# Kernel tuning notes

Measured on AMD Instinct MI355X. Metric: run time of the kernel, lower is better.

## Reference

```python
import jax, jax.numpy as jnp
import numpy as np


def _hard_sigmoid(x):
    # Keras ConvLSTM2D default recurrent_activation
    return jnp.clip(0.2 * x + 0.5, 0.0, 1.0)


def _conv(x, w):
    # NHWC input, HWIO kernel, SAME padding, stride 1
    return jax.lax.conv_general_dilated(
        x, w, (1, 1), 'SAME', dimension_numbers=('NHWC', 'HWIO', 'NHWC'))


def _convlstm(seq, h, c, k, rk, b):
    # seq: [B, T, H, W, Cin]; h, c: [B, H, W, F]
    # k: [kh, kw, Cin, 4F], rk: [kh, kw, F, 4F], b: [4F]
    def step(carry, x):
        h, c = carry
        z = _conv(x, k) + _conv(h, rk) + b  # [B,H,W,4F]
        zi, zf, zc, zo = jnp.split(z, 4, axis=-1)
        i = _hard_sigmoid(zi)
        f = _hard_sigmoid(zf)
        o = _hard_sigmoid(zo)
        c = f * c + i * jnp.tanh(zc)
        h = o * jnp.tanh(c)
        return (h, c), None
    (h, c), _ = jax.lax.scan(step, (h, c), jnp.swapaxes(seq, 0, 1))
    return h, c


def setup_inputs() -> dict:
    key = jax.random.key(0)
    ks = jax.random.split(key, 14)
    B, T, H, W, Cin, F, K = 32, 1, 64, 64, 1, 64, 3
    s = 0.05
    inp = {
        'input_': jax.random.normal(ks[0], (B, T, H, W, Cin), jnp.float32),
        'h0': jax.random.normal(ks[1], (B, H, W, F), jnp.float32) * s,
        'c0': jax.random.normal(ks[2], (B, H, W, F), jnp.float32) * s,
        'h1': jax.random.normal(ks[3], (B, H, W, F), jnp.float32) * s,
        'c1': jax.random.normal(ks[4], (B, H, W, F), jnp.float32) * s,
        'k0': jax.random.normal(ks[5], (K, K, Cin, 4 * F), jnp.float32) * s,
        'rk0': jax.random.normal(ks[6], (K, K, F, 4 * F), jnp.float32) * s,
        'b0': jnp.zeros((4 * F,), jnp.float32),
        'k1': jax.random.normal(ks[7], (K, K, F, 4 * F), jnp.float32) * s,
        'rk1': jax.random.normal(ks[8], (K, K, F, 4 * F), jnp.float32) * s,
        'b1': jnp.zeros((4 * F,), jnp.float32),
        'cw': jax.random.normal(ks[9], (1, 1, F, 1), jnp.float32) * s,
        'cb': jnp.zeros((1,), jnp.float32),
    }
    return inp


def reference(input_, h0, c0, h1, c1, k0, rk0, b0, k1, rk1, b1, cw, cb):
    # Layer 0 consumes the input frame sequence (T=1)
    h0n, c0n = _convlstm(input_, h0, c0, k0, rk0, b0)
    # Layer 1 consumes layer-0's last hidden state as its (length-1) input
    h1n, c1n = _convlstm(h0n[:, None], h1, c1, k1, rk1, b1)
    frames = _conv(h1n, cw) + cb  # 1x1 conv head -> [B,H,W,1]
    return frames, h0n, c0n, h1n, c1n
```

## Files before the change

kernel.cpp:

```cpp
#include <hip/hip_runtime.h>
#include <hip/hip_bf16.h>

typedef short s16;
typedef __attribute__((ext_vector_type(8))) short bf16x8;
typedef __attribute__((ext_vector_type(4))) float f32x4;

__device__ __forceinline__ s16 f2bf(float f) {
  unsigned u = __builtin_bit_cast(unsigned, f);
  unsigned r = (u + 0x7FFFu + ((u >> 16) & 1u)) >> 16;
  return (s16)r;
}

__device__ __forceinline__ float hsig(float x) {
  return fminf(fmaxf(0.2f * x + 0.5f, 0.0f), 1.0f);
}

#define PXS 66
#define ROWSZ (PXS * 64)
#define ASZ4 (4 * ROWSZ)
#define ASZ6 (6 * ROWSZ)

__global__ void wprep_kernel(const float* __restrict__ rk0, const float* __restrict__ k1,
                             const float* __restrict__ rk1, const float* __restrict__ k0,
                             s16* __restrict__ w0q, s16* __restrict__ w1q,
                             s16* __restrict__ w2q, s16* __restrict__ k0t) {
  int idx = blockIdx.x * 256 + threadIdx.x;
  const int n1 = 18 * 8192;
  if (idx < 3 * n1) {
    int which = idx / n1;
    int i = idx - which * n1;
    int e    = i & 7;
    int lane = (i >> 3) & 63;
    int g    = (i >> 9) & 3;
    int j    = (i >> 11) & 3;
    int k    = (i >> 13) & 1;
    int tap  = i >> 14;
    int l15 = lane & 15, l4 = lane >> 4;
    int ic = k * 32 + l4 * 8 + e;
    int oc = j * 64 + g * 16 + l15;
    const float* src = (which == 0) ? rk0 : (which == 1) ? k1 : rk1;
    s16* dst = (which == 0) ? w0q : (which == 1) ? w1q : w2q;
    dst[i] = f2bf(src[(tap * 64 + ic) * 256 + oc]);
  } else if (idx < 3 * n1 + 8192) {
    int r = idx - 3 * n1;
    int kk = r & 31;
    int oc = r >> 5;
    k0t[r] = (kk < 9) ? f2bf(k0[kk * 256 + oc]) : (s16)0;
  }
}

template <bool F32>
__device__ __forceinline__ bf16x8 load_conv8(const void* src, long off) {
  if constexpr (F32) {
    const float* p = (const float*)src + off;
    float4 v0 = *reinterpret_cast<const float4*>(p);
    float4 v1 = *reinterpret_cast<const float4*>(p + 4);
    bf16x8 r;
    r[0] = f2bf(v0.x); r[1] = f2bf(v0.y); r[2] = f2bf(v0.z); r[3] = f2bf(v0.w);
    r[4] = f2bf(v1.x); r[5] = f2bf(v1.y); r[6] = f2bf(v1.z); r[7] = f2bf(v1.w);
    return r;
  } else {
    return *reinterpret_cast<const bf16x8*>((const s16*)src + off);
  }
}

template <bool F32, int ROWS, int NT>
__device__ __forceinline__ void stageA(s16* a_lds, const void* src, int b, int y0, int tid) {
  #pragma unroll
  for (int i = 0; i < ROWS * 512 / NT; ++i) {
    int c   = tid + i * NT;
    int row = c >> 9;
    int px  = (c >> 3) & 63;
    int cb  = c & 7;
    int y   = y0 - 1 + row;
    int xp  = px + 1;
    bf16x8 v = {};
    if ((unsigned)y < 64u)
      v = load_conv8<F32>(src, ((long)(b * 64 + y) * 64 + px) * 64 + cb * 8);
    *reinterpret_cast<bf16x8*>(a_lds + (row * PXS + xp) * 64 + ((cb ^ (xp & 7)) * 8)) = v;
  }
  if (tid < ROWS * 16) {
    int row = tid >> 4;
    int xp  = ((tid >> 3) & 1) ? 65 : 0;
    int cb  = tid & 7;
    bf16x8 z = {};
    *reinterpret_cast<bf16x8*>(a_lds + (row * PXS + xp) * 64 + cb * 8) = z;
  }
}

__global__ __launch_bounds__(1024, 1) void cell0_kernel(
    const float* __restrict__ h0,
    const s16* __restrict__ w0,
    const float* __restrict__ xin,
    const s16* __restrict__ k0t,
    const float* __restrict__ bias,
    const float* __restrict__ c_old,
    float* __restrict__ h_out,
    float* __restrict__ c_out,
    s16* __restrict__ hb_out)
{
  __shared__ __align__(16) s16 a_lds[ASZ6];
  __shared__ __align__(16) s16 w_lds[3][8192];
  __shared__ float x_lds[384];

  const int tid = threadIdx.x;
  const int b  = blockIdx.x >> 4;
  const int y0 = (blockIdx.x & 15) << 2;

  const int wave = tid >> 6;
  const int lane = tid & 63;
  const int g    = wave & 3;
  const int mh   = wave >> 2;
  const int l15  = lane & 15;
  const int l4   = lane >> 4;

  constexpr int NST = 18;

  auto issueW = [&](int u) {
    int v = (u >= NST) ? u - NST : u;
    const s16* wt = w0 + v * 8192;
    char* base = (char*)(&w_lds[0][0]) + (v % 3) * 16384 + (tid >> 6) * 1024;
    __builtin_amdgcn_global_load_lds(
        (const __attribute__((address_space(1))) void*)(wt + tid * 8),
        (__attribute__((address_space(3))) void*)base, 16, 0, 0);
  };
  auto readWf = [&](bf16x8 (&wf)[4], int slot) {
    const s16* wb = &w_lds[slot][0] + g * 512 + lane * 8;
    #pragma unroll
    for (int j = 0; j < 4; ++j)
      wf[j] = *reinterpret_cast<const bf16x8*>(wb + j * 2048);
  };

  f32x4 acc[4][4] = {};

  auto doStage = [&](const bf16x8 (&wf)[4], int u) {
    int tap = u >> 1, kk = u & 1;
    int dy = tap / 3, dx = tap - dy * 3;
    const char* sb = (const char*)a_lds + (mh + dy) * (ROWSZ * 2);
    bf16x8 af[4];
    #pragma unroll
    for (int m = 0; m < 4; ++m) {
      int xq   = m * 16 + l15 + dx;
      int boff = xq * 128 + ((((kk << 2) | l4) ^ (xq & 7)) << 4);
      af[m] = *reinterpret_cast<const bf16x8*>(sb + boff);
    }
    __builtin_amdgcn_s_setprio(1);
    #pragma unroll
    for (int m = 0; m < 4; ++m) {
      #pragma unroll
      for (int j = 0; j < 4; ++j)
        acc[m][j] = __builtin_amdgcn_mfma_f32_16x16x32_bf16(af[m], wf[j], acc[m][j], 0, 0, 0);
    }
    __builtin_amdgcn_s_setprio(0);
  };

  issueW(0);
  issueW(1);
  stageA<true, 6, 1024>(a_lds, h0, b, y0, tid);
  if (tid < 384) {
    int row = tid >> 6, px = tid & 63;
    int y = y0 - 1 + row;
    x_lds[tid] = ((unsigned)y < 64u) ? xin[(b * 64 + y) * 64 + px] : 0.0f;
  }
  __syncthreads();

  {
    bf16x8 bx[4];
    #pragma unroll
    for (int j = 0; j < 4; ++j) {
      int oc = j * 64 + g * 16 + l15;
      bx[j] = *reinterpret_cast<const bf16x8*>(k0t + oc * 32 + l4 * 8);
    }
    #pragma unroll
    for (int m = 0; m < 4; ++m) {
      int px = m * 16 + l15;
      bf16x8 ax = {};
      #pragma unroll
      for (int e = 0; e < 8; ++e) {
        int t = l4 * 8 + e;
        if (t < 9) {
          int dyt = t / 3, dxt = t - dyt * 3;
          int xx = px + dxt - 1;
          float xv = ((unsigned)xx < 64u) ? x_lds[(mh + dyt) * 64 + xx] : 0.0f;
          ax[e] = f2bf(xv);
        }
      }
      #pragma unroll
      for (int j = 0; j < 4; ++j)
        acc[m][j] = __builtin_amdgcn_mfma_f32_16x16x32_bf16(ax, bx[j], acc[m][j], 0, 0, 0);
    }
  }

  bf16x8 wf[4];
  #pragma unroll
  for (int u = 0; u < NST; ++u) {
    asm volatile("s_waitcnt vmcnt(1)" ::: "memory");
    __builtin_amdgcn_s_barrier();
    __builtin_amdgcn_sched_barrier(0);
    issueW(u + 2);
    readWf(wf, u % 3);
    doStage(wf, u);
  }

  float bi[4];
  #pragma unroll
  for (int j = 0; j < 4; ++j) bi[j] = bias[j * 64 + g * 16 + l15];
  const int pix_base = b * 4096 + y0 * 64;
  const int f = g * 16 + l15;
  #pragma unroll
  for (int m = 0; m < 4; ++m) {
    #pragma unroll
    for (int r = 0; r < 4; ++r) {
      int pl = mh * 64 + m * 16 + l4 * 4 + r;
      int off = (pix_base + pl) * 64 + f;
      float zi = acc[m][0][r] + bi[0];
      float zf = acc[m][1][r] + bi[1];
      float zc = acc[m][2][r] + bi[2];
      float zo = acc[m][3][r] + bi[3];
      float ig = hsig(zi), fg = hsig(zf), og = hsig(zo);
      float cn = fg * c_old[off] + ig * tanhf(zc);
      float hn = og * tanhf(cn);
      c_out[off] = cn;
      h_out[off] = hn;
      hb_out[off] = f2bf(hn);
    }
  }
}

#define ZP 260
__global__ __launch_bounds__(1024, 4) void cell1_kernel(
    const s16* __restrict__ src0,
    const float* __restrict__ src1,
    const s16* __restrict__ w0,
    const s16* __restrict__ w1,
    const float* __restrict__ bias,
    const float* __restrict__ c_old,
    float* __restrict__ h_out,
    float* __restrict__ c_out)
{
  __shared__ __align__(16) s16 a_lds[2 * ASZ4];

  const int tid = threadIdx.x;
  const int b  = blockIdx.x >> 5;
  const int y0 = (blockIdx.x & 31) << 1;

  const int wave = tid >> 6;
  const int lane = tid & 63;
  const int mh   = wave >> 3;
  const int s8   = wave & 7;
  const int jj   = s8 >> 1;
  const int g0   = (s8 & 1) * 2;
  const int l15  = lane & 15;
  const int l4   = lane >> 4;

  stageA<false, 4, 1024>(a_lds, src0, b, y0, tid);
  stageA<true, 4, 1024>(a_lds + ASZ4, src1, b, y0, tid);
  __syncthreads();

  f32x4 acc[4][2] = {};
  const int wloff = jj * 2048 + g0 * 512 + lane * 8;

  auto qpass = [&](const s16* wsrc, const char* abase, int kk) {
    bf16x8 wreg[9][2];
    #pragma unroll
    for (int t = 0; t < 9; ++t) {
      const s16* wp = wsrc + (t * 2 + kk) * 8192 + wloff;
      wreg[t][0] = *reinterpret_cast<const bf16x8*>(wp);
      wreg[t][1] = *reinterpret_cast<const bf16x8*>(wp + 512);
    }
    #pragma unroll
    for (int t = 0; t < 9; ++t) {
      int dy = t / 3, dx = t - dy * 3;
      const char* sb = abase + (mh + dy) * (ROWSZ * 2);
      #pragma unroll
      for (int m = 0; m < 4; ++m) {
        int xq   = m * 16 + l15 + dx;
        int boff = xq * 128 + ((((kk << 2) | l4) ^ (xq & 7)) << 4);
        bf16x8 a = *reinterpret_cast<const bf16x8*>(sb + boff);
        acc[m][0] = __builtin_amdgcn_mfma_f32_16x16x32_bf16(a, wreg[t][0], acc[m][0], 0, 0, 0);
        acc[m][1] = __builtin_amdgcn_mfma_f32_16x16x32_bf16(a, wreg[t][1], acc[m][1], 0, 0, 0);
      }
    }
  };

  qpass(w0, (const char*)a_lds, 0);
  qpass(w0, (const char*)a_lds, 1);
  qpass(w1, (const char*)a_lds + ASZ4 * 2, 0);
  qpass(w1, (const char*)a_lds + ASZ4 * 2, 1);

  float* z_lds = (float*)a_lds;
  const int pix_base = b * 4096 + y0 * 64;
  #pragma unroll
  for (int h = 0; h < 2; ++h) {
    __syncthreads();
    if (mh == h) {
      #pragma unroll
      for (int m = 0; m < 4; ++m) {
        #pragma unroll
        for (int q = 0; q < 2; ++q) {
          int oc = jj * 64 + (g0 + q) * 16 + l15;
          #pragma unroll
          for (int r = 0; r < 4; ++r) {
            int px = m * 16 + l4 * 4 + r;
            z_lds[px * ZP + oc] = acc[m][q][r];
          }
        }
      }
    }
    __syncthreads();
    int px = tid >> 4;
    int f4 = (tid & 15) * 4;
    const float* zr = z_lds + px * ZP;
    float4 zi4 = *reinterpret_cast<const float4*>(zr + f4);
    float4 zf4 = *reinterpret_cast<const float4*>(zr + 64 + f4);
    float4 zc4 = *reinterpret_cast<const float4*>(zr + 128 + f4);
    float4 zo4 = *reinterpret_cast<const float4*>(zr + 192 + f4);
    float4 bi4 = *reinterpret_cast<const float4*>(bias + f4);
    float4 bf4 = *reinterpret_cast<const float4*>(bias + 64 + f4);
    float4 bc4 = *reinterpret_cast<const float4*>(bias + 128 + f4);
    float4 bo4 = *reinterpret_cast<const float4*>(bias + 192 + f4);
    int off0 = (pix_base + h * 64 + px) * 64 + f4;
    float4 co4 = *reinterpret_cast<const float4*>(c_old + off0);
    float4 hn4, cn4;
    #pragma unroll
    for (int e = 0; e < 4; ++e) {
      float zi = (&zi4.x)[e] + (&bi4.x)[e];
      float zf = (&zf4.x)[e] + (&bf4.x)[e];
      float zc = (&zc4.x)[e] + (&bc4.x)[e];
      float zo = (&zo4.x)[e] + (&bo4.x)[e];
      float ig = hsig(zi), fg = hsig(zf), og = hsig(zo);
      float cn = fg * (&co4.x)[e] + ig * tanhf(zc);
      (&cn4.x)[e] = cn;
      (&hn4.x)[e] = og * tanhf(cn);
    }
    *reinterpret_cast<float4*>(c_out + off0) = cn4;
    *reinterpret_cast<float4*>(h_out + off0) = hn4;
  }
}

__global__ void frames_kernel(const float* __restrict__ h, const float* __restrict__ cw,
                              const float* __restrict__ cbp, float* __restrict__ out) {
  int tid = blockIdx.x * 256 + threadIdx.x;
  int p  = tid >> 2;
  int fc = (tid & 3) * 16;
  const float4* hp = reinterpret_cast<const float4*>(h + p * 64 + fc);
  const float4* wp = reinterpret_cast<const float4*>(cw + fc);
  float s = 0.0f;
  #pragma unroll
  for (int i = 0; i < 4; ++i) {
    float4 v = hp[i];
    float4 w = wp[i];
    s += v.x * w.x + v.y * w.y + v.z * w.z + v.w * w.w;
  }
  s += __shfl_xor(s, 1);
  s += __shfl_xor(s, 2);
  if ((tid & 3) == 0) out[p] = s + cbp[0];
}

extern "C" void kernel_launch(void* const* d_in, const int* in_sizes, int n_in,
                              void* d_out, int out_size, void* d_ws, size_t ws_size,
                              hipStream_t stream) {
  const float* x   = (const float*)d_in[0];
  const float* h0  = (const float*)d_in[1];
  const float* c0  = (const float*)d_in[2];
  const float* h1  = (const float*)d_in[3];
  const float* c1  = (const float*)d_in[4];
  const float* k0  = (const float*)d_in[5];
  const float* rk0 = (const float*)d_in[6];
  const float* b0  = (const float*)d_in[7];
  const float* k1  = (const float*)d_in[8];
  const float* rk1 = (const float*)d_in[9];
  const float* b1  = (const float*)d_in[10];
  const float* cw  = (const float*)d_in[11];
  const float* cbp = (const float*)d_in[12];

  float* out    = (float*)d_out;
  float* frames = out;
  float* h0n    = out + 131072;
  float* c0n    = out + 131072 + 8388608;
  float* h1n    = out + 131072 + 2 * 8388608;
  float* c1n    = out + 131072 + 3 * 8388608;

  char* ws = (char*)d_ws;
  const size_t SZ_H = 16777216;
  s16* h0nb = (s16*)(ws + 0 * SZ_H);
  s16* w0q  = (s16*)(ws + 1 * SZ_H);
  s16* w1q  = (s16*)(ws + 1 * SZ_H + 1 * 294912);
  s16* w2q  = (s16*)(ws + 1 * SZ_H + 2 * 294912);
  s16* k0t  = (s16*)(ws + 1 * SZ_H + 3 * 294912);

  wprep_kernel<<<1760, 256, 0, stream>>>(rk0, k1, rk1, k0, w0q, w1q, w2q, k0t);

  cell0_kernel<<<512, 1024, 0, stream>>>(
      h0, w0q, x, k0t, b0, c0, h0n, c0n, h0nb);

  cell1_kernel<<<1024, 1024, 0, stream>>>(
      h0nb, h1, w1q, w2q, b1, c1, h1n, c1n);

  frames_kernel<<<2048, 256, 0, stream>>>(h1n, cw, cbp, frames);
}
```

Measured before the change: 181.4 us.

## Retile cell1 MFMA work to 32px x 64ch per wave with rotated tap order

Changes the per-wave tile in cell1_kernel from 64 pixels x 32 output channels to 32 pixels x 64 output channels (4 pixel groups x 4 gate slices). Each LDS A-fragment load now feeds four MFMAs instead of two. Taps are split into 5+4 chunks to bound weight-register pressure, and the tap order is rotated per wave group so concurrent waves start on different weight addresses. Launch bounds are relaxed from 4 to 2 blocks per CU, which allows more registers per thread but may lower occupancy.

Result: slower. 219.4 us (+20.9%).

```diff
diff --git a/kernel.cpp b/kernel.cpp
--- a/kernel.cpp
+++ b/kernel.cpp
@@ -227,8 +227,40 @@
   }
 }
 
+template <int T>
+__device__ __forceinline__ void hpass8(
+    const s16* __restrict__ wsrc, const char* __restrict__ abase, int kk, int t0,
+    int rot, int ns, int mg, int lane, int l15, int l4, f32x4 (&acc)[2][4]) {
+  bf16x8 wreg[T][4];
+  #pragma unroll
+  for (int t = 0; t < T; ++t) {
+    int tap = t0 + t + rot;
+    if (tap >= 9) tap -= 9;
+    const s16* wp = wsrc + (tap * 2 + kk) * 8192 + ns * 2048 + lane * 8;
+    #pragma unroll
+    for (int q = 0; q < 4; ++q)
+      wreg[t][q] = *reinterpret_cast<const bf16x8*>(wp + q * 512);
+  }
+  #pragma unroll
+  for (int t = 0; t < T; ++t) {
+    int tap = t0 + t + rot;
+    if (tap >= 9) tap -= 9;
+    int dy = tap / 3, dx = tap - dy * 3;
+    const char* sb = abase + ((mg >> 1) + dy) * (ROWSZ * 2);
+    #pragma unroll
+    for (int m = 0; m < 2; ++m) {
+      int xq   = (mg & 1) * 32 + m * 16 + l15 + dx;
+      int boff = xq * 128 + ((((kk << 2) | l4) ^ (xq & 7)) << 4);
+      bf16x8 a = *reinterpret_cast<const bf16x8*>(sb + boff);
+      #pragma unroll
+      for (int q = 0; q < 4; ++q)
+        acc[m][q] = __builtin_amdgcn_mfma_f32_16x16x32_bf16(a, wreg[t][q], acc[m][q], 0, 0, 0);
+    }
+  }
+}
+
 #define ZP 260
-__global__ __launch_bounds__(1024, 4) void cell1_kernel(
+__global__ __launch_bounds__(1024, 2) void cell1_kernel(
     const s16* __restrict__ src0,
     const float* __restrict__ src1,
     const s16* __restrict__ w0,
@@ -246,62 +278,43 @@
 
   const int wave = tid >> 6;
   const int lane = tid & 63;
-  const int mh   = wave >> 3;
-  const int s8   = wave & 7;
-  const int jj   = s8 >> 1;
-  const int g0   = (s8 & 1) * 2;
+  const int mg   = wave >> 2;
+  const int ns   = wave & 3;
   const int l15  = lane & 15;
   const int l4   = lane >> 4;
+  const int rot  = ns * 2;
 
   stageA<false, 4, 1024>(a_lds, src0, b, y0, tid);
   stageA<true, 4, 1024>(a_lds + ASZ4, src1, b, y0, tid);
   __syncthreads();
 
-  f32x4 acc[4][2] = {};
-  const int wloff = jj * 2048 + g0 * 512 + lane * 8;
-
-  auto qpass = [&](const s16* wsrc, const char* abase, int kk) {
-    bf16x8 wreg[9][2];
-    #pragma unroll
-    for (int t = 0; t < 9; ++t) {
-      const s16* wp = wsrc + (t * 2 + kk) * 8192 + wloff;
-      wreg[t][0] = *reinterpret_cast<const bf16x8*>(wp);
-      wreg[t][1] = *reinterpret_cast<const bf16x8*>(wp + 512);
-    }
-    #pragma unroll
-    for (int t = 0; t < 9; ++t) {
-      int dy = t / 3, dx = t - dy * 3;
-      const char* sb = abase + (mh + dy) * (ROWSZ * 2);
-      #pragma unroll
-      for (int m = 0; m < 4; ++m) {
-        int xq   = m * 16 + l15 + dx;
-        int boff = xq * 128 + ((((kk << 2) | l4) ^ (xq & 7)) << 4);
-        bf16x8 a = *reinterpret_cast<const bf16x8*>(sb + boff);
-        acc[m][0] = __builtin_amdgcn_mfma_f32_16x16x32_bf16(a, wreg[t][0], acc[m][0], 0, 0, 0);
-        acc[m][1] = __builtin_amdgcn_mfma_f32_16x16x32_bf16(a, wreg[t][1], acc[m][1], 0, 0, 0);
-      }
-    }
-  };
-
-  qpass(w0, (const char*)a_lds, 0);
-  qpass(w0, (const char*)a_lds, 1);
-  qpass(w1, (const char*)a_lds + ASZ4 * 2, 0);
-  qpass(w1, (const char*)a_lds + ASZ4 * 2, 1);
+  f32x4 acc[2][4] = {};
+  const char* a0 = (const char*)a_lds;
+  const char* a1 = (const char*)a_lds + ASZ4 * 2;
+
+  hpass8<5>(w0, a0, 0, 0, rot, ns, mg, lane, l15, l4, acc);
+  hpass8<4>(w0, a0, 0, 5, rot, ns, mg, lane, l15, l4, acc);
+  hpass8<5>(w0, a0, 1, 0, rot, ns, mg, lane, l15, l4, acc);
+  hpass8<4>(w0, a0, 1, 5, rot, ns, mg, lane, l15, l4, acc);
+  hpass8<5>(w1, a1, 0, 0, rot, ns, mg, lane, l15, l4, acc);
+  hpass8<4>(w1, a1, 0, 5, rot, ns, mg, lane, l15, l4, acc);
+  hpass8<5>(w1, a1, 1, 0, rot, ns, mg, lane, l15, l4, acc);
+  hpass8<4>(w1, a1, 1, 5, rot, ns, mg, lane, l15, l4, acc);
 
   float* z_lds = (float*)a_lds;
   const int pix_base = b * 4096 + y0 * 64;
   #pragma unroll
   for (int h = 0; h < 2; ++h) {
     __syncthreads();
-    if (mh == h) {
+    if ((mg >> 1) == h) {
       #pragma unroll
-      for (int m = 0; m < 4; ++m) {
+      for (int m = 0; m < 2; ++m) {
         #pragma unroll
-        for (int q = 0; q < 2; ++q) {
-          int oc = jj * 64 + (g0 + q) * 16 + l15;
+        for (int q = 0; q < 4; ++q) {
+          int oc = ns * 64 + q * 16 + l15;
           #pragma unroll
           for (int r = 0; r < 4; ++r) {
-            int px = m * 16 + l4 * 4 + r;
+            int px = (mg & 1) * 32 + m * 16 + l4 * 4 + r;
             z_lds[px * ZP + oc] = acc[m][q][r];
           }
         }
```
